# Performance work log

Measured on AMD Instinct MI355X. Metric: run time of the kernel, lower is better.

Reference implementation:

```python
import jax, jax.numpy as jnp
import numpy as np

B, S, DIM = 2, 2048, 2048
H = 16
Q_RANK, KV_RANK = 512, 512
D_NOPE, D_ROPE, D_V = 128, 64, 128
D_QK = D_NOPE + D_ROPE  # 192
EPS = 1e-6
SCALE = D_QK ** -0.5


def setup_inputs() -> dict:
    key = jax.random.key(0)
    ks = jax.random.split(key, 8)
    x = jax.random.normal(ks[0], (B, S, DIM), dtype=jnp.float32)
    # real RoPE table: theta_i = 10000^{-2i/d}, angles = pos * theta
    inv_freq = 1.0 / (10000.0 ** (np.arange(0, D_ROPE, 2, dtype=np.float32) / D_ROPE))
    ang = np.arange(S, dtype=np.float32)[:, None] * inv_freq[None, :]  # (S, D_ROPE//2)
    freqs_cis = jnp.asarray(np.stack([np.cos(ang), np.sin(ang)], axis=-1))  # (S, 32, 2)
    std = 0.02
    wq_a = jax.random.normal(ks[1], (Q_RANK, DIM), dtype=jnp.float32) * std
    wq_b = jax.random.normal(ks[2], (H * D_QK, Q_RANK), dtype=jnp.float32) * std
    wkv_a = jax.random.normal(ks[3], (KV_RANK + D_ROPE, DIM), dtype=jnp.float32) * std
    wkv_b = jax.random.normal(ks[4], (H * (D_NOPE + D_V), KV_RANK), dtype=jnp.float32) * std
    wo = jax.random.normal(ks[5], (DIM, H * D_V), dtype=jnp.float32) * std
    q_norm_w = jnp.ones((Q_RANK,), dtype=jnp.float32)
    kv_norm_w = jnp.ones((KV_RANK,), dtype=jnp.float32)
    return {"x": x, "freqs_cis": freqs_cis, "wq_a": wq_a, "wq_b": wq_b,
            "q_norm_w": q_norm_w, "wkv_a": wkv_a, "kv_norm_w": kv_norm_w,
            "wkv_b": wkv_b, "wo": wo}


def _rmsnorm(x, w):
    var = jnp.mean(jnp.square(x), axis=-1, keepdims=True)
    return x * jax.lax.rsqrt(var + EPS) * w


def _rope(x, freqs_cis):
    # x: (B, S, h, d); freqs_cis: (S, d//2, 2) as (cos, sin). Pairs are interleaved (x0,x1),(x2,x3),...
    xr, xi = x[..., 0::2], x[..., 1::2]
    cos = freqs_cis[None, :, None, :, 0]
    sin = freqs_cis[None, :, None, :, 1]
    yr = xr * cos - xi * sin
    yi = xr * sin + xi * cos
    return jnp.stack([yr, yi], axis=-1).reshape(x.shape)


def reference(x, freqs_cis, wq_a, wq_b, q_norm_w, wkv_a, kv_norm_w, wkv_b, wo):
    b, s, _ = x.shape
    # low-rank Q projection: wq_a -> RMSNorm -> wq_b
    q = _rmsnorm(x @ wq_a.T, q_norm_w) @ wq_b.T
    q = q.reshape(b, s, H, D_QK)
    q_nope, q_pe = q[..., :D_NOPE], q[..., D_NOPE:]
    q = jnp.concatenate([q_nope, _rope(q_pe, freqs_cis)], axis=-1)  # (b,s,H,192)
    # KV path
    kv = x @ wkv_a.T  # (b,s,KV_RANK+D_ROPE)
    kv_lat, k_pe = kv[..., :KV_RANK], kv[..., KV_RANK:]
    k_pe = _rope(k_pe[:, :, None, :], freqs_cis)  # (b,s,1,64)
    kv = (_rmsnorm(kv_lat, kv_norm_w) @ wkv_b.T).reshape(b, s, H, D_NOPE + D_V)
    k_nope, v = kv[..., :D_NOPE], kv[..., D_NOPE:]
    k = jnp.concatenate([k_nope, jnp.broadcast_to(k_pe, (b, s, H, D_ROPE))], axis=-1)
    # causal scaled-dot-product attention
    scores = jnp.einsum('bshd,bthd->bhst', q, k) * SCALE
    mask = jnp.tril(jnp.ones((s, s), dtype=bool))
    scores = jnp.where(mask[None, None], scores, jnp.finfo(scores.dtype).min)
    probs = jax.nn.softmax(scores, axis=-1)
    out = jnp.einsum('bhst,bthd->bshd', probs, v).reshape(b, s, H * D_V)
    return out @ wo.T
```

## Files before the change

### kernel.cpp

```cpp
#include <hip/hip_runtime.h>
#include <cstdint>
#include <cstddef>


typedef unsigned short u16;
typedef unsigned int u32;
typedef unsigned long long u64;
typedef __attribute__((ext_vector_type(8))) short bf16x8;
typedef __attribute__((ext_vector_type(4))) float floatx4;

#define MFMA16x16x32 __builtin_amdgcn_mfma_f32_16x16x32_bf16

#define QSCALE 0.10411755f
#define THR_L2 11.541560f

__device__ __forceinline__ u16 f2bf(float f) {
  u32 u = __float_as_uint(f);
  u32 r = (u + 0x7fffu + ((u >> 16) & 1u)) >> 16;
  return (u16)r;
}
__device__ __forceinline__ float bf2f(u16 b) {
  return __uint_as_float(((u32)b) << 16);
}
__device__ __forceinline__ u32 cvtpk(float lo, float hi) {
  u32 r;
  asm("v_cvt_pk_bf16_f32 %0, %1, %2" : "=v"(r) : "v"(lo), "v"(hi));
  return r;
}
__device__ __forceinline__ void gload16(const void* g, void* l) {
  __builtin_amdgcn_global_load_lds(
      (const __attribute__((address_space(1))) void*)g,
      (__attribute__((address_space(3))) void*)l, 16, 0, 0);
}

__global__ __launch_bounds__(256) void cvt_all(
    const float* __restrict__ s0, const float* __restrict__ s1,
    const float* __restrict__ s2, const float* __restrict__ s3,
    const float* __restrict__ s4, const float* __restrict__ s5,
    u16* __restrict__ d0, u16* __restrict__ d1, u16* __restrict__ d2,
    u16* __restrict__ d3, u16* __restrict__ d4, u16* __restrict__ d5) {
  constexpr int ST1 = 2097152;
  constexpr int ST2 = ST1 + 262144;
  constexpr int ST3 = ST2 + 294912;
  constexpr int ST4 = ST3 + 393216;
  constexpr int ST5 = ST4 + 524288;
  constexpr int TOT = ST5 + 1048576;
  int i = blockIdx.x * 256 + threadIdx.x;
  int stride = gridDim.x * 256;
  for (; i < TOT; i += stride) {
    const float* sp;
    u16* dp;
    int j;
    if (i < ST1)      { sp = s0; dp = d0; j = i; }
    else if (i < ST2) { sp = s1; dp = d1; j = i - ST1; }
    else if (i < ST3) { sp = s2; dp = d2; j = i - ST2; }
    else if (i < ST4) { sp = s3; dp = d3; j = i - ST3; }
    else if (i < ST5) { sp = s4; dp = d4; j = i - ST4; }
    else              { sp = s5; dp = d5; j = i - ST5; }
    float4 v = ((const float4*)sp)[j];
    ushort4 o;
    o.x = f2bf(v.x); o.y = f2bf(v.y); o.z = f2bf(v.z); o.w = f2bf(v.w);
    ((ushort4*)dp)[j] = o;
  }
}

template <int BM, int BN, bool OBF16>
__global__ __launch_bounds__(512) void gemm8(const u16* __restrict__ A,
                                             const u16* __restrict__ B,
                                             void* __restrict__ Cv,
                                             int M, int N, int K) {
  constexpr int WM = BM / 2;
  constexpr int AF = WM / 16;
  constexpr int LA = BM * 4 / 512;
  constexpr int LB = BN * 4 / 512;
  constexpr int S = LA + LB;
  __shared__ alignas(16) u16 As[2][BM * 32];
  __shared__ alignas(16) u16 Bs[2][BN * 32];
  const int m0 = blockIdx.y * BM, n0 = blockIdx.x * BN;
  const int t = threadIdx.x;
  const int wv = t >> 6, lane = t & 63, g = lane >> 4, qq = lane & 15;
  const int wr = wv >> 2, wc = wv & 3;
  const int fsw = (qq >> 1) & 3;
  size_t aoff[LA], boff[LB];
#pragma unroll
  for (int i = 0; i < LA; ++i) {
    int seg = t + i * 512;
    int row = seg >> 2, sl = seg & 3;
    aoff[i] = (size_t)(m0 + row) * K + (sl ^ ((row >> 1) & 3)) * 8;
  }
#pragma unroll
  for (int i = 0; i < LB; ++i) {
    int seg = t + i * 512;
    int row = seg >> 2, sl = seg & 3;
    boff[i] = (size_t)(n0 + row) * K + (sl ^ ((row >> 1) & 3)) * 8;
  }
  const floatx4 fz = {0.f, 0.f, 0.f, 0.f};
  floatx4 acc[AF][4];
#pragma unroll
  for (int m = 0; m < AF; ++m)
#pragma unroll
    for (int n = 0; n < 4; ++n) acc[m][n] = fz;

#define GS8(buf, k0)                                                          \
  {                                                                           \
    _Pragma("unroll") for (int i = 0; i < LA; ++i)                            \
        gload16(&A[aoff[i] + (k0)], &As[buf][(size_t)(wv * 64 + i * 512) * 8]); \
    _Pragma("unroll") for (int i = 0; i < LB; ++i)                            \
        gload16(&B[boff[i] + (k0)], &Bs[buf][(size_t)(wv * 64 + i * 512) * 8]); \
  }

  const int nk = K >> 5;
  GS8(0, 0);
  GS8(1, 32);
  for (int kt = 0; kt < nk; ++kt) {
    asm volatile("" ::: "memory");
    if (kt + 1 < nk) {
      if constexpr (S == 4)
        asm volatile("s_waitcnt vmcnt(4)" ::: "memory");
      else
        asm volatile("s_waitcnt vmcnt(3)" ::: "memory");
    } else {
      asm volatile("s_waitcnt vmcnt(0)" ::: "memory");
    }
    __builtin_amdgcn_s_barrier();
    asm volatile("" ::: "memory");
    const u16* Ab = &As[kt & 1][0];
    const u16* Bb = &Bs[kt & 1][0];
    bf16x8 af[AF], bfr[4];
#pragma unroll
    for (int m = 0; m < AF; ++m)
      af[m] = *(const bf16x8*)&Ab[(wr * WM + m * 16 + qq) * 32 + ((g ^ fsw) * 8)];
#pragma unroll
    for (int n = 0; n < 4; ++n)
      bfr[n] = *(const bf16x8*)&Bb[(wc * 64 + n * 16 + qq) * 32 + ((g ^ fsw) * 8)];
    asm volatile("s_waitcnt lgkmcnt(0)" ::: "memory");
    __builtin_amdgcn_s_barrier();
    asm volatile("" ::: "memory");
    if (kt + 2 < nk) GS8(kt & 1, (kt + 2) * 32);
    __builtin_amdgcn_s_setprio(1);
#pragma unroll
    for (int m = 0; m < AF; ++m)
#pragma unroll
      for (int n = 0; n < 4; ++n)
        acc[m][n] = MFMA16x16x32(af[m], bfr[n], acc[m][n], 0, 0, 0);
    __builtin_amdgcn_s_setprio(0);
  }
#undef GS8
#pragma unroll
  for (int m = 0; m < AF; ++m)
#pragma unroll
    for (int n = 0; n < 4; ++n)
#pragma unroll
      for (int r = 0; r < 4; ++r) {
        int row = m0 + wr * WM + m * 16 + 4 * g + r;
        int col = n0 + wc * 64 + n * 16 + qq;
        if constexpr (OBF16)
          ((u16*)Cv)[(size_t)row * N + col] = f2bf(acc[m][n][r]);
        else
          ((float*)Cv)[(size_t)row * N + col] = acc[m][n][r];
      }
}

__global__ __launch_bounds__(256) void rmsnorm_bf16(const float* __restrict__ in,
                                                    int stride,
                                                    const float* __restrict__ w,
                                                    u16* __restrict__ out) {
  const int row = blockIdx.x, t = threadIdx.x;
  __shared__ float wsum[4];
  float2 v = *(const float2*)&in[(size_t)row * stride + 2 * t];
  float ss = v.x * v.x + v.y * v.y;
#pragma unroll
  for (int off = 1; off < 64; off <<= 1) ss += __shfl_xor(ss, off);
  if ((t & 63) == 0) wsum[t >> 6] = ss;
  __syncthreads();
  float tot = wsum[0] + wsum[1] + wsum[2] + wsum[3];
  float r = rsqrtf(tot * (1.f / 512.f) + 1e-6f);
  out[(size_t)row * 512 + 2 * t] = f2bf(v.x * r * w[2 * t]);
  out[(size_t)row * 512 + 2 * t + 1] = f2bf(v.y * r * w[2 * t + 1]);
}

__global__ __launch_bounds__(256) void rope_kpe(const float* __restrict__ ap,
                                                const float* __restrict__ fc,
                                                u16* __restrict__ kpe) {
  int idx = blockIdx.x * 256 + threadIdx.x;
  int row = idx >> 5, j = idx & 31;
  int s = row & 2047;
  float xr = ap[(size_t)row * 1280 + 1024 + 2 * j];
  float xi = ap[(size_t)row * 1280 + 1024 + 2 * j + 1];
  float c = fc[(s * 32 + j) * 2], sn = fc[(s * 32 + j) * 2 + 1];
  u32 lo = f2bf(xr * c - xi * sn), hi = f2bf(xr * sn + xi * c);
  *(u32*)&kpe[(size_t)row * 64 + 2 * j] = lo | (hi << 16);
}

__global__ __launch_bounds__(256) void rope_pack_q(const u16* __restrict__ qf,
                                                   const float* __restrict__ fc,
                                                   u16* __restrict__ qbf) {
  int idx = blockIdx.x * 256 + threadIdx.x;
  int j = idx % 96;
  int rh = idx / 96;
  int h = rh & 15, row = rh >> 4;
  int b = row >> 11, s = row & 2047;
  const u16* src = qf + (size_t)row * 3072 + h * 192;
  u16* dst = qbf + ((size_t)(b * 16 + h) * 2048 + s) * 192;
  if (j < 64) {
    u32 w = *(const u32*)&src[2 * j];
    u32 lo = f2bf(bf2f((u16)w) * QSCALE);
    u32 hi = f2bf(bf2f((u16)(w >> 16)) * QSCALE);
    *(u32*)&dst[2 * j] = lo | (hi << 16);
  } else {
    int jp = j - 64;
    u32 w = *(const u32*)&src[128 + 2 * jp];
    float xr = bf2f((u16)w), xi = bf2f((u16)(w >> 16));
    float c = fc[(s * 32 + jp) * 2], sn = fc[(s * 32 + jp) * 2 + 1];
    u32 lo = f2bf((xr * c - xi * sn) * QSCALE);
    u32 hi = f2bf((xr * sn + xi * c) * QSCALE);
    *(u32*)&dst[128 + 2 * jp] = lo | (hi << 16);
  }
}

__global__ __launch_bounds__(256) void pack_k(const u16* __restrict__ kvb,
                                              const u16* __restrict__ kpe,
                                              u16* __restrict__ kbf) {
  int idx = blockIdx.x * 256 + threadIdx.x;
  int j = idx % 96;
  int rh = idx / 96;
  int h = rh & 15, row = rh >> 4;
  int b = row >> 11, s = row & 2047;
  u16* dst = kbf + ((size_t)(b * 16 + h) * 2048 + s) * 192;
  if (j < 64) {
    *(u32*)&dst[2 * j] = *(const u32*)&kvb[(size_t)row * 4096 + h * 256 + 2 * j];
  } else {
    int jp = j - 64;
    *(u32*)&dst[128 + 2 * jp] = *(const u32*)&kpe[(size_t)row * 64 + 2 * jp];
  }
}

__global__ __launch_bounds__(256) void transpose_v(const u16* __restrict__ kvb,
                                                   u16* __restrict__ vt) {
  __shared__ u16 T[32][34];
  const int bh = blockIdx.z, b = bh >> 4, h = bh & 15;
  const int s0 = blockIdx.x * 32, d0 = blockIdx.y * 32;
  const int tx = threadIdx.x & 31, ty = threadIdx.x >> 5;
#pragma unroll
  for (int i = 0; i < 4; ++i) {
    int sl = ty + i * 8;
    T[sl][tx] = kvb[(size_t)(b * 2048 + s0 + sl) * 4096 + h * 256 + 128 + d0 + tx];
  }
  __syncthreads();
#pragma unroll
  for (int i = 0; i < 4; ++i) {
    int dl = ty + i * 8;
    vt[((size_t)bh * 128 + d0 + dl) * 2048 + s0 + tx] = T[tx][dl];
  }
}

__global__ __launch_bounds__(256, 4) void flash_attn(const u16* __restrict__ Q,
                                                     const u16* __restrict__ Kc,
                                                     const u16* __restrict__ VT,
                                                     u16* __restrict__ O) {
  __shared__ alignas(16) u16 Ks[2][32 * 192];
  __shared__ alignas(16) u16 Vs[2][128 * 32];
  const int bid = blockIdx.x;
  const int qt = 31 - (bid >> 5);
  const int bh = bid & 31;
  const int t = threadIdx.x, wv = t >> 6, lane = t & 63;
  const int g = lane >> 4, qq = lane & 15;
  const int qrow0 = qt * 64 + wv * 16;
  const int my_last = qrow0 + 15;
  const int q_glob = qrow0 + qq;
  const int nkt = 2 * qt + 2;

  int koffg[3], voffg[2];
#pragma unroll
  for (int i = 0; i < 3; ++i) {
    int seg = t + i * 256;
    int row = seg / 24, sl = seg - row * 24;
    koffg[i] = row * 192 + (sl ^ ((row >> 1) & 7)) * 8;
  }
#pragma unroll
  for (int i = 0; i < 2; ++i) {
    int seg = t + i * 256;
    int row = seg >> 2, sl = seg & 3;
    voffg[i] = row * 2048 + (sl ^ ((row >> 1) & 3)) * 8;
  }
  const u16* Kt0 = Kc + (size_t)bh * 2048 * 192;
  const u16* Vt0 = VT + (size_t)bh * 128 * 2048;

  bf16x8 qf[6];
  {
    const u16* qp = Q + ((size_t)bh * 2048 + qrow0 + qq) * 192;
#pragma unroll
    for (int kk = 0; kk < 6; ++kk) qf[kk] = *(const bf16x8*)&qp[kk * 32 + g * 8];
  }
  asm volatile("s_waitcnt vmcnt(0)" ::: "memory");

  const floatx4 fz = {0.f, 0.f, 0.f, 0.f};
  floatx4 oacc[8];
  floatx4 oacc_l = fz;
#pragma unroll
  for (int d = 0; d < 8; ++d) oacc[d] = fz;
  float m_run = -1e30f;

  bf16x8 ones;
#pragma unroll
  for (int i = 0; i < 8; ++i) ones[i] = (short)0x3f80;

  const int krow0 = 2 * qq;
  const int krow1 = 2 * qq + 1;
  const int xrk = qq & 7;
  const int vsw = (qq >> 1) & 3;

#define STAGE(buf, kt)                                                       \
  {                                                                          \
    const u16* Kg = Kt0 + (size_t)(kt) * (32 * 192);                         \
    const u16* Vg = Vt0 + (kt) * 32;                                         \
    _Pragma("unroll") for (int i = 0; i < 3; ++i)                            \
        gload16(Kg + koffg[i], &Ks[buf][(size_t)(wv * 64 + i * 256) * 8]);   \
    _Pragma("unroll") for (int i = 0; i < 2; ++i)                            \
        gload16(Vg + voffg[i], &Vs[buf][(size_t)(wv * 64 + i * 256) * 8]);   \
  }

  STAGE(0, 0);
  for (int kt = 0; kt < nkt; ++kt) {
    const int k0 = kt * 32;
    asm volatile("" ::: "memory");
    if (kt + 1 < nkt) {
      STAGE((kt + 1) & 1, kt + 1);
      asm volatile("s_waitcnt vmcnt(5)" ::: "memory");
    } else {
      asm volatile("s_waitcnt vmcnt(0)" ::: "memory");
    }
    __builtin_amdgcn_s_barrier();
    asm volatile("" ::: "memory");
    if (k0 <= my_last) {
      const u16* Kb = &Ks[kt & 1][0];
      const u16* Vb = &Vs[kt & 1][0];
      floatx4 s0 = fz, s1 = fz;
      __builtin_amdgcn_s_setprio(1);
#pragma unroll
      for (int kk = 0; kk < 6; ++kk) {
        int sl = kk * 4 + g;
        bf16x8 a0 = *(const bf16x8*)&Kb[krow0 * 192 + ((sl ^ xrk) * 8)];
        bf16x8 a1 = *(const bf16x8*)&Kb[krow1 * 192 + ((sl ^ xrk) * 8)];
        s0 = MFMA16x16x32(a0, qf[kk], s0, 0, 0, 0);
        s1 = MFMA16x16x32(a1, qf[kk], s1, 0, 0, 0);
      }
      __builtin_amdgcn_s_setprio(0);
      float v[8];
      if (k0 + 31 <= qrow0) {
#pragma unroll
        for (int r = 0; r < 4; ++r) {
          v[r] = s0[r];
          v[4 + r] = s1[r];
        }
      } else {
#pragma unroll
        for (int r = 0; r < 4; ++r) {
          int key0 = k0 + 8 * g + 2 * r;
          v[r] = (key0 <= q_glob) ? s0[r] : -1e30f;
          v[4 + r] = (key0 + 1 <= q_glob) ? s1[r] : -1e30f;
        }
      }
      float mloc = fmaxf(fmaxf(fmaxf(v[0], v[1]), fmaxf(v[2], v[3])),
                         fmaxf(fmaxf(v[4], v[5]), fmaxf(v[6], v[7])));
      if (!__all(mloc <= m_run + THR_L2)) {
        float mx = fmaxf(mloc, __shfl_xor(mloc, 16));
        mx = fmaxf(mx, __shfl_xor(mx, 32));
        float m_new = fmaxf(m_run, mx);
        float alpha = exp2f(m_run - m_new);
        m_run = m_new;
#pragma unroll
        for (int d = 0; d < 8; ++d)
#pragma unroll
          for (int r = 0; r < 4; ++r) oacc[d][r] *= alpha;
#pragma unroll
        for (int r = 0; r < 4; ++r) oacc_l[r] *= alpha;
      }
      float pex[8];
#pragma unroll
      for (int i = 0; i < 8; ++i) pex[i] = exp2f(v[i] - m_run);
      bf16x8 pf;
      ((u32*)&pf)[0] = cvtpk(pex[0], pex[4]);
      ((u32*)&pf)[1] = cvtpk(pex[1], pex[5]);
      ((u32*)&pf)[2] = cvtpk(pex[2], pex[6]);
      ((u32*)&pf)[3] = cvtpk(pex[3], pex[7]);
      __builtin_amdgcn_s_setprio(1);
#pragma unroll
      for (int d = 0; d < 8; ++d) {
        bf16x8 vf = *(const bf16x8*)&Vb[(d * 16 + qq) * 32 + ((g ^ vsw) * 8)];
        oacc[d] = MFMA16x16x32(vf, pf, oacc[d], 0, 0, 0);
      }
      oacc_l = MFMA16x16x32(ones, pf, oacc_l, 0, 0, 0);
      __builtin_amdgcn_s_setprio(0);
    }
    asm volatile("" ::: "memory");
    __builtin_amdgcn_s_barrier();
  }
#undef STAGE
  float linv = 1.f / oacc_l[0];
  const int b = bh >> 4, h = bh & 15;
  size_t rowoff = ((size_t)b * 2048 + qrow0 + qq) * 2048 + h * 128 + 4 * g;
#pragma unroll
  for (int d = 0; d < 8; ++d) {
    u32 lo = cvtpk(oacc[d][0] * linv, oacc[d][1] * linv);
    u32 hi = cvtpk(oacc[d][2] * linv, oacc[d][3] * linv);
    u64 w = (u64)lo | ((u64)hi << 32);
    *(u64*)&O[rowoff + d * 16] = w;
  }
}

extern "C" void kernel_launch(void* const* d_in, const int* in_sizes, int n_in,
                              void* d_out, int out_size, void* d_ws,
                              size_t ws_size, hipStream_t stream) {
  (void)in_sizes; (void)n_in; (void)out_size;
  const float* x = (const float*)d_in[0];
  const float* fc = (const float*)d_in[1];
  const float* wqa = (const float*)d_in[2];
  const float* wqb = (const float*)d_in[3];
  const float* qnw = (const float*)d_in[4];
  const float* wkva = (const float*)d_in[5];
  const float* kvnw = (const float*)d_in[6];
  const float* wkvb = (const float*)d_in[7];
  const float* wo = (const float*)d_in[8];
  float* out = (float*)d_out;
  char* ws = (char*)d_ws;

  size_t off = 0;
  auto alloc = [&](size_t bytes) {
    size_t o = off;
    off += (bytes + 255) & ~(size_t)255;
    return o;
  };
  const size_t o_xbf = alloc(16777216);
  const size_t o_wa = alloc(5242880);
  const size_t o_wqb = alloc(3145728);
  const size_t o_wkvb = alloc(4194304);
  const size_t o_wo = alloc(8388608);
  const size_t o_qln = alloc(4194304);
  const size_t o_kvln = alloc(4194304);
  const size_t o_kpe = alloc(524288);
  const size_t o_big = alloc(33554432);
  const size_t o_qbf = alloc(25165824);
  const size_t o_kbf = alloc(25165824);
  const size_t o_vt = alloc(16777216);
  if (ws_size < off) return;

  u16* xbf = (u16*)(ws + o_xbf);
  u16* wab = (u16*)(ws + o_wa);
  u16* wqbb = (u16*)(ws + o_wqb);
  u16* wkvbb = (u16*)(ws + o_wkvb);
  u16* wob = (u16*)(ws + o_wo);
  u16* qlatn = (u16*)(ws + o_qln);
  u16* kvlatn = (u16*)(ws + o_kvln);
  u16* kpe = (u16*)(ws + o_kpe);
  float* aproj = (float*)(ws + o_big);
  u16* qfb = (u16*)(ws + o_big);
  u16* kvbb = (u16*)(ws + o_big);
  u16* qbf = (u16*)(ws + o_qbf);
  u16* kbf = (u16*)(ws + o_kbf);
  u16* vt = (u16*)(ws + o_vt);
  u16* attnbf = (u16*)(ws + o_xbf);

  cvt_all<<<2048, 256, 0, stream>>>(x, wqa, wkva, wqb, wkvb, wo,
                                    xbf, wab, wab + 1048576, wqbb, wkvbb, wob);

  gemm8<128, 256, false><<<dim3(5, 32), 512, 0, stream>>>(
      xbf, wab, aproj, 4096, 1280, 2048);
  rmsnorm_bf16<<<4096, 256, 0, stream>>>(aproj, 1280, qnw, qlatn);
  rmsnorm_bf16<<<4096, 256, 0, stream>>>(aproj + 512, 1280, kvnw, kvlatn);
  rope_kpe<<<512, 256, 0, stream>>>(aproj, fc, kpe);

  gemm8<256, 256, true><<<dim3(12, 16), 512, 0, stream>>>(
      qlatn, wqbb, qfb, 4096, 3072, 512);
  rope_pack_q<<<24576, 256, 0, stream>>>(qfb, fc, qbf);

  gemm8<256, 256, true><<<dim3(16, 16), 512, 0, stream>>>(
      kvlatn, wkvbb, kvbb, 4096, 4096, 512);
  pack_k<<<24576, 256, 0, stream>>>(kvbb, kpe, kbf);
  transpose_v<<<dim3(64, 4, 32), 256, 0, stream>>>(kvbb, vt);

  flash_attn<<<1024, 256, 0, stream>>>(qbf, kbf, vt, attnbf);
  gemm8<128, 256, false><<<dim3(8, 32), 512, 0, stream>>>(
      attnbf, wob, out, 4096, 2048, 2048);
}
```

Measured before the change: 289.5 us.

## Fuse RoPE, Q/K packing and V transpose into GEMM epilogues

Moves the Q RoPE and scale, the K head-major packing and the V transpose into specialized epilogues of the projection GEMMs, writing straight into the attention layouts. This removes the rope_pack_q, pack_k and transpose_v kernels and their intermediate buffer round trips. The first projection now stores bf16 instead of fp32, which adds a rounding step before RMSNorm and the k_pe RoPE, and the k_pe RoPE result is broadcast into every head slot of K directly. The epilogues use lane shuffles and scattered 4- and 8-byte stores, which may coalesce less well than the old row-major stores.

```diff
diff --git a/kernel.cpp b/kernel.cpp
--- a/kernel.cpp
+++ b/kernel.cpp
@@ -64,11 +64,13 @@
   }
 }
 
-template <int BM, int BN, bool OBF16>
+template <int BM, int BN, int EPI>
 __global__ __launch_bounds__(512) void gemm8(const u16* __restrict__ A,
                                              const u16* __restrict__ B,
                                              void* __restrict__ Cv,
-                                             int M, int N, int K) {
+                                             int M, int N, int K,
+                                             const float* __restrict__ fcp,
+                                             void* __restrict__ aux) {
   constexpr int WM = BM / 2;
   constexpr int AF = WM / 16;
   constexpr int LA = BM * 4 / 512;
@@ -146,112 +148,104 @@
     __builtin_amdgcn_s_setprio(0);
   }
 #undef GS8
+
 #pragma unroll
   for (int m = 0; m < AF; ++m)
 #pragma unroll
-    for (int n = 0; n < 4; ++n)
-#pragma unroll
-      for (int r = 0; r < 4; ++r) {
-        int row = m0 + wr * WM + m * 16 + 4 * g + r;
-        int col = n0 + wc * 64 + n * 16 + qq;
-        if constexpr (OBF16)
-          ((u16*)Cv)[(size_t)row * N + col] = f2bf(acc[m][n][r]);
-        else
-          ((float*)Cv)[(size_t)row * N + col] = acc[m][n][r];
+    for (int n = 0; n < 4; ++n) {
+      const int col16 = n0 + wc * 64 + n * 16;
+      if constexpr (EPI == 0 || EPI == 1) {
+#pragma unroll
+        for (int r = 0; r < 4; ++r) {
+          int row = m0 + wr * WM + m * 16 + 4 * g + r;
+          int col = col16 + qq;
+          if constexpr (EPI == 1)
+            ((u16*)Cv)[(size_t)row * N + col] = f2bf(acc[m][n][r]);
+          else
+            ((float*)Cv)[(size_t)row * N + col] = acc[m][n][r];
+        }
+      } else if constexpr (EPI == 2) {
+        const int h = col16 / 192;
+        const int jb = col16 - h * 192 + qq;
+#pragma unroll
+        for (int r = 0; r < 4; ++r) {
+          int row = m0 + wr * WM + m * 16 + 4 * g + r;
+          int b = row >> 11, s = row & 2047;
+          float own = acc[m][n][r];
+          float par = __shfl_xor(own, 1);
+          if ((qq & 1) == 0) {
+            u32 w;
+            if (jb < 128) {
+              w = cvtpk(own * QSCALE, par * QSCALE);
+            } else {
+              int jp = (jb - 128) >> 1;
+              float c = fcp[(s * 32 + jp) * 2];
+              float sn = fcp[(s * 32 + jp) * 2 + 1];
+              w = cvtpk((own * c - par * sn) * QSCALE,
+                        (own * sn + par * c) * QSCALE);
+            }
+            *(u32*)((u16*)Cv + ((size_t)(b * 16 + h) * 2048 + s) * 192 + jb) = w;
+          }
+        }
+      } else {
+        const int h = col16 >> 8;
+        const int jb = (col16 & 255) + qq;
+        if (jb < 128) {
+#pragma unroll
+          for (int r = 0; r < 4; ++r) {
+            int row = m0 + wr * WM + m * 16 + 4 * g + r;
+            int b = row >> 11, s = row & 2047;
+            float own = acc[m][n][r];
+            float par = __shfl_xor(own, 1);
+            if ((qq & 1) == 0)
+              *(u32*)((u16*)Cv + ((size_t)(b * 16 + h) * 2048 + s) * 192 + jb) =
+                  cvtpk(own, par);
+          }
+        } else {
+          int row0 = m0 + wr * WM + m * 16 + 4 * g;
+          int b = row0 >> 11, s0v = row0 & 2047;
+          int dv = jb - 128;
+          u32 lo = cvtpk(acc[m][n][0], acc[m][n][1]);
+          u32 hi = cvtpk(acc[m][n][2], acc[m][n][3]);
+          u64 w = (u64)lo | ((u64)hi << 32);
+          *(u64*)((u16*)aux + ((size_t)(b * 16 + h) * 128 + dv) * 2048 + s0v) = w;
+        }
       }
-}
-
-__global__ __launch_bounds__(256) void rmsnorm_bf16(const float* __restrict__ in,
-                                                    int stride,
-                                                    const float* __restrict__ w,
-                                                    u16* __restrict__ out) {
+    }
+}
+
+__global__ __launch_bounds__(256) void rmsnorm_u16(const u16* __restrict__ in,
+                                                   int stride,
+                                                   const float* __restrict__ w,
+                                                   u16* __restrict__ out) {
   const int row = blockIdx.x, t = threadIdx.x;
   __shared__ float wsum[4];
-  float2 v = *(const float2*)&in[(size_t)row * stride + 2 * t];
-  float ss = v.x * v.x + v.y * v.y;
+  u32 wv2 = *(const u32*)&in[(size_t)row * stride + 2 * t];
+  float vx = bf2f((u16)wv2), vy = bf2f((u16)(wv2 >> 16));
+  float ss = vx * vx + vy * vy;
 #pragma unroll
   for (int off = 1; off < 64; off <<= 1) ss += __shfl_xor(ss, off);
   if ((t & 63) == 0) wsum[t >> 6] = ss;
   __syncthreads();
   float tot = wsum[0] + wsum[1] + wsum[2] + wsum[3];
   float r = rsqrtf(tot * (1.f / 512.f) + 1e-6f);
-  out[(size_t)row * 512 + 2 * t] = f2bf(v.x * r * w[2 * t]);
-  out[(size_t)row * 512 + 2 * t + 1] = f2bf(v.y * r * w[2 * t + 1]);
-}
-
-__global__ __launch_bounds__(256) void rope_kpe(const float* __restrict__ ap,
-                                                const float* __restrict__ fc,
-                                                u16* __restrict__ kpe) {
+  *(u32*)&out[(size_t)row * 512 + 2 * t] =
+      cvtpk(vx * r * w[2 * t], vy * r * w[2 * t + 1]);
+}
+
+__global__ __launch_bounds__(256) void rope_kpe_bcast(const u16* __restrict__ ap,
+                                                      const float* __restrict__ fc,
+                                                      u16* __restrict__ kbf) {
   int idx = blockIdx.x * 256 + threadIdx.x;
   int row = idx >> 5, j = idx & 31;
-  int s = row & 2047;
-  float xr = ap[(size_t)row * 1280 + 1024 + 2 * j];
-  float xi = ap[(size_t)row * 1280 + 1024 + 2 * j + 1];
+  int b = row >> 11, s = row & 2047;
+  u32 wv2 = *(const u32*)&ap[(size_t)row * 1280 + 1024 + 2 * j];
+  float xr = bf2f((u16)wv2), xi = bf2f((u16)(wv2 >> 16));
   float c = fc[(s * 32 + j) * 2], sn = fc[(s * 32 + j) * 2 + 1];
-  u32 lo = f2bf(xr * c - xi * sn), hi = f2bf(xr * sn + xi * c);
-  *(u32*)&kpe[(size_t)row * 64 + 2 * j] = lo | (hi << 16);
-}
-
-__global__ __launch_bounds__(256) void rope_pack_q(const u16* __restrict__ qf,
-                                                   const float* __restrict__ fc,
-                                                   u16* __restrict__ qbf) {
-  int idx = blockIdx.x * 256 + threadIdx.x;
-  int j = idx % 96;
-  int rh = idx / 96;
-  int h = rh & 15, row = rh >> 4;
-  int b = row >> 11, s = row & 2047;
-  const u16* src = qf + (size_t)row * 3072 + h * 192;
-  u16* dst = qbf + ((size_t)(b * 16 + h) * 2048 + s) * 192;
-  if (j < 64) {
-    u32 w = *(const u32*)&src[2 * j];
-    u32 lo = f2bf(bf2f((u16)w) * QSCALE);
-    u32 hi = f2bf(bf2f((u16)(w >> 16)) * QSCALE);
-    *(u32*)&dst[2 * j] = lo | (hi << 16);
-  } else {
-    int jp = j - 64;
-    u32 w = *(const u32*)&src[128 + 2 * jp];
-    float xr = bf2f((u16)w), xi = bf2f((u16)(w >> 16));
-    float c = fc[(s * 32 + jp) * 2], sn = fc[(s * 32 + jp) * 2 + 1];
-    u32 lo = f2bf((xr * c - xi * sn) * QSCALE);
-    u32 hi = f2bf((xr * sn + xi * c) * QSCALE);
-    *(u32*)&dst[128 + 2 * jp] = lo | (hi << 16);
-  }
-}
-
-__global__ __launch_bounds__(256) void pack_k(const u16* __restrict__ kvb,
-                                              const u16* __restrict__ kpe,
-                                              u16* __restrict__ kbf) {
-  int idx = blockIdx.x * 256 + threadIdx.x;
-  int j = idx % 96;
-  int rh = idx / 96;
-  int h = rh & 15, row = rh >> 4;
-  int b = row >> 11, s = row & 2047;
-  u16* dst = kbf + ((size_t)(b * 16 + h) * 2048 + s) * 192;
-  if (j < 64) {
-    *(u32*)&dst[2 * j] = *(const u32*)&kvb[(size_t)row * 4096 + h * 256 + 2 * j];
-  } else {
-    int jp = j - 64;
-    *(u32*)&dst[128 + 2 * jp] = *(const u32*)&kpe[(size_t)row * 64 + 2 * jp];
-  }
-}
-
-__global__ __launch_bounds__(256) void transpose_v(const u16* __restrict__ kvb,
-                                                   u16* __restrict__ vt) {
-  __shared__ u16 T[32][34];
-  const int bh = blockIdx.z, b = bh >> 4, h = bh & 15;
-  const int s0 = blockIdx.x * 32, d0 = blockIdx.y * 32;
-  const int tx = threadIdx.x & 31, ty = threadIdx.x >> 5;
-#pragma unroll
-  for (int i = 0; i < 4; ++i) {
-    int sl = ty + i * 8;
-    T[sl][tx] = kvb[(size_t)(b * 2048 + s0 + sl) * 4096 + h * 256 + 128 + d0 + tx];
-  }
-  __syncthreads();
-#pragma unroll
-  for (int i = 0; i < 4; ++i) {
-    int dl = ty + i * 8;
-    vt[((size_t)bh * 128 + d0 + dl) * 2048 + s0 + tx] = T[tx][dl];
-  }
+  u32 w = cvtpk(xr * c - xi * sn, xr * sn + xi * c);
+#pragma unroll
+  for (int h = 0; h < 16; ++h)
+    *(u32*)&kbf[((size_t)(b * 16 + h) * 2048 + s) * 192 + 128 + 2 * j] = w;
 }
 
 __global__ __launch_bounds__(256, 4) void flash_attn(const u16* __restrict__ Q,
@@ -438,8 +432,7 @@
   const size_t o_wo = alloc(8388608);
   const size_t o_qln = alloc(4194304);
   const size_t o_kvln = alloc(4194304);
-  const size_t o_kpe = alloc(524288);
-  const size_t o_big = alloc(33554432);
+  const size_t o_ap = alloc(10485760);
   const size_t o_qbf = alloc(25165824);
   const size_t o_kbf = alloc(25165824);
   const size_t o_vt = alloc(16777216);
@@ -452,10 +445,7 @@
   u16* wob = (u16*)(ws + o_wo);
   u16* qlatn = (u16*)(ws + o_qln);
   u16* kvlatn = (u16*)(ws + o_kvln);
-  u16* kpe = (u16*)(ws + o_kpe);
-  float* aproj = (float*)(ws + o_big);
-  u16* qfb = (u16*)(ws + o_big);
-  u16* kvbb = (u16*)(ws + o_big);
+  u16* ap = (u16*)(ws + o_ap);
   u16* qbf = (u16*)(ws + o_qbf);
   u16* kbf = (u16*)(ws + o_kbf);
   u16* vt = (u16*)(ws + o_vt);
@@ -464,22 +454,19 @@
   cvt_all<<<2048, 256, 0, stream>>>(x, wqa, wkva, wqb, wkvb, wo,
                                     xbf, wab, wab + 1048576, wqbb, wkvbb, wob);
 
-  gemm8<128, 256, false><<<dim3(5, 32), 512, 0, stream>>>(
-      xbf, wab, aproj, 4096, 1280, 2048);
-  rmsnorm_bf16<<<4096, 256, 0, stream>>>(aproj, 1280, qnw, qlatn);
-  rmsnorm_bf16<<<4096, 256, 0, stream>>>(aproj + 512, 1280, kvnw, kvlatn);
-  rope_kpe<<<512, 256, 0, stream>>>(aproj, fc, kpe);
-
-  gemm8<256, 256, true><<<dim3(12, 16), 512, 0, stream>>>(
-      qlatn, wqbb, qfb, 4096, 3072, 512);
-  rope_pack_q<<<24576, 256, 0, stream>>>(qfb, fc, qbf);
-
-  gemm8<256, 256, true><<<dim3(16, 16), 512, 0, stream>>>(
-      kvlatn, wkvbb, kvbb, 4096, 4096, 512);
-  pack_k<<<24576, 256, 0, stream>>>(kvbb, kpe, kbf);
-  transpose_v<<<dim3(64, 4, 32), 256, 0, stream>>>(kvbb, vt);
+  gemm8<128, 256, 1><<<dim3(5, 32), 512, 0, stream>>>(
+      xbf, wab, ap, 4096, 1280, 2048, nullptr, nullptr);
+  rmsnorm_u16<<<4096, 256, 0, stream>>>(ap, 1280, qnw, qlatn);
+  rmsnorm_u16<<<4096, 256, 0, stream>>>(ap + 512, 1280, kvnw, kvlatn);
+  rope_kpe_bcast<<<512, 256, 0, stream>>>(ap, fc, kbf);
+
+  gemm8<256, 256, 2><<<dim3(12, 16), 512, 0, stream>>>(
+      qlatn, wqbb, qbf, 4096, 3072, 512, fc, nullptr);
+
+  gemm8<256, 256, 3><<<dim3(16, 16), 512, 0, stream>>>(
+      kvlatn, wkvbb, kbf, 4096, 4096, 512, nullptr, vt);
 
   flash_attn<<<1024, 256, 0, stream>>>(qbf, kbf, vt, attnbf);
-  gemm8<128, 256, false><<<dim3(8, 32), 512, 0, stream>>>(
-      attnbf, wob, out, 4096, 2048, 2048);
-}
+  gemm8<128, 256, 0><<<dim3(8, 32), 512, 0, stream>>>(
+      attnbf, wob, out, 4096, 2048, 2048, nullptr, nullptr);
+}
```

New measurement: 288.2 us. No clear change (-0.4%).
